# Performance work log

Hardware: AMD Instinct MI355X
Metric: run time of the kernel (lower is better)

Reference implementation:

```python
import jax, jax.numpy as jnp
import numpy as np

B, S, HID, NH = 2, 2048, 1024, 16
HD = HID // NH
BASE = 10000.0


def _rope_tables(seq_len, head_dim):
    i = jnp.arange(0, head_dim, 2, dtype=jnp.float32)
    theta = BASE ** (-i / head_dim)
    pos = jnp.arange(seq_len, dtype=jnp.float32)
    m_theta = jnp.outer(pos, theta)  # [S, HD/2]
    cos = jnp.repeat(jnp.cos(m_theta), 2, axis=1)  # [S, HD]
    sin = jnp.repeat(jnp.sin(m_theta), 2, axis=1)
    return cos, sin


def _apply_rope(x, cos, sin):
    # x: [B, NH, S, HD]; interleaved rotation: (-x1, x0, -x3, x2, ...)
    x_even = x[..., 0::2]
    x_odd = x[..., 1::2]
    inv_x = jnp.stack((-x_odd, x_even), axis=-1).reshape(x.shape)
    return x * cos[None, None] + inv_x * sin[None, None]


def setup_inputs() -> dict:
    key = jax.random.key(0)
    ks = jax.random.split(key, 7)
    q = jax.random.normal(ks[0], (B, S, HID), dtype=jnp.float32)
    k = jax.random.normal(ks[1], (B, S, HID), dtype=jnp.float32)
    v = jax.random.normal(ks[2], (B, S, HID), dtype=jnp.float32)
    scale = 1.0 / np.sqrt(HID)
    Wq = jax.random.normal(ks[3], (HID, HID), dtype=jnp.float32) * scale
    Wk = jax.random.normal(ks[4], (HID, HID), dtype=jnp.float32) * scale
    Wv = jax.random.normal(ks[5], (HID, HID), dtype=jnp.float32) * scale
    Wo = jax.random.normal(ks[6], (HID, HID), dtype=jnp.float32) * scale
    mask = jnp.triu(jnp.ones((S, S), dtype=bool), k=1)[None, None]  # causal, True = masked
    return {"q": q, "k": k, "v": v, "mask": mask,
            "Wq": Wq, "Wk": Wk, "Wv": Wv, "Wo": Wo}


def reference(q, k, v, mask, Wq, Wk, Wv, Wo):
    cos, sin = _rope_tables(S, HD)
    # Linear (torch stores weight as [out, in]; y = x @ W.T)
    qh = (q @ Wq.T).reshape(B, S, NH, HD).transpose(0, 2, 1, 3)
    kh = (k @ Wk.T).reshape(B, S, NH, HD).transpose(0, 2, 1, 3)
    vh = (v @ Wv.T).reshape(B, S, NH, HD).transpose(0, 2, 1, 3)
    qh = _apply_rope(qh, cos, sin)
    kh = _apply_rope(kh, cos, sin)
    scores = jnp.einsum("bhqd,bhkd->bhqk", qh, kh) / np.sqrt(HD)
    neg_min = jnp.finfo(jnp.float32).min
    scores = jnp.where(mask, neg_min, scores)
    attn = jax.nn.softmax(scores, axis=-1)
    out = jnp.einsum("bhqk,bhkd->bhqd", attn, vh)  # [B,NH,S,HD]
    out = out.transpose(0, 2, 1, 3).reshape(B, S, HID)
    return out @ Wo.T
```

## Files before the change

kernel.cpp:

```cpp
#include <hip/hip_runtime.h>

#define S_LEN 2048
#define HIDN  1024
#define NHEAD 16
#define HDIM  64
#define MROWS 4096
#define KDIM  1024
#define NDIM  1024

typedef __attribute__((ext_vector_type(8))) short bf16x8;
typedef __attribute__((ext_vector_type(4))) short bf16x4;
typedef __attribute__((ext_vector_type(4))) float f32x4;

static __device__ __forceinline__ ushort f2bf(float f) {
    unsigned int u = __float_as_uint(f);
    u = (u + 0x7fffu + ((u >> 16) & 1u)) >> 16;
    return (ushort)u;
}
static __device__ __forceinline__ float bf2f(ushort u) {
    return __uint_as_float(((unsigned int)u) << 16);
}

static __device__ __forceinline__ void gload16(const ushort* g, ushort* l) {
    __builtin_amdgcn_global_load_lds(
        (const __attribute__((address_space(1))) unsigned int*)g,
        (__attribute__((address_space(3))) unsigned int*)l, 16, 0, 0);
}

__global__ __launch_bounds__(256) void prep_kernel(
    const float* __restrict__ q, const float* __restrict__ k,
    const float* __restrict__ v, const float* __restrict__ Wq,
    const float* __restrict__ Wk, const float* __restrict__ Wv,
    const float* __restrict__ Wo,
    ushort* __restrict__ qb, ushort* __restrict__ kb, ushort* __restrict__ vb,
    ushort* __restrict__ Wqb, ushort* __restrict__ Wkb, ushort* __restrict__ Wvb,
    ushort* __restrict__ Wob,
    float* __restrict__ rc, float* __restrict__ rs)
{
    const long Q4 = (long)MROWS * KDIM / 4;
    const long W4 = (long)NDIM * KDIM / 4;
    if (blockIdx.x < 16384) {
        long i = (long)blockIdx.x * 256 + threadIdx.x;
        const float* src; ushort* dst; long off;
        if (i < Q4)          { src = q; dst = qb; off = i; }
        else if (i < 2 * Q4) { src = k; dst = kb; off = i - Q4; }
        else if (i < 3 * Q4) { src = v; dst = vb; off = i - 2 * Q4; }
        else {
            long t = i - 3 * Q4;
            int wsel = (int)(t >> 18);
            off = t & (W4 - 1);
            src = (wsel == 0) ? Wq : (wsel == 1) ? Wk : (wsel == 2) ? Wv : Wo;
            dst = (wsel == 0) ? Wqb : (wsel == 1) ? Wkb : (wsel == 2) ? Wvb : Wob;
        }
        float4 vv = ((const float4*)src)[off];
        ushort4 o;
        o.x = f2bf(vv.x); o.y = f2bf(vv.y); o.z = f2bf(vv.z); o.w = f2bf(vv.w);
        ((ushort4*)dst)[off] = o;
    } else {
        int idx = (blockIdx.x - 16384) * 256 + threadIdx.x;
        int s  = idx >> 5;
        int jp = idx & 31;
        float theta = expf(-(float)(2 * jp) * (9.210340371976184f / 64.0f));
        float ang = (float)s * theta;
        float sv, cv;
        sincosf(ang, &sv, &cv);
        rc[idx] = cv;
        rs[idx] = sv;
    }
}

static __device__ __forceinline__ void gemm_mainloop(
    const ushort* __restrict__ A, const ushort* __restrict__ W,
    ushort* As, ushort* Bs, f32x4 (&acc)[2][4],
    int m0, int n0, int tid)
{
    const int lane = tid & 63, wid = tid >> 6;
    const int wm = wid & 1, wn = wid >> 1;
    const int quad = lane >> 4, l15 = lane & 15;

    for (int k0 = 0; k0 < KDIM; k0 += 64) {
        __syncthreads();
#pragma unroll
        for (int rr = 0; rr < 2; ++rr) {
            int sidx = tid + rr * 256;
            int row = sidx >> 3;
            int g = (sidx & 7) ^ (row & 7);
            gload16(A + (size_t)(m0 + row) * KDIM + k0 + g * 8, As + sidx * 8);
        }
#pragma unroll
        for (int rr = 0; rr < 4; ++rr) {
            int sidx = tid + rr * 256;
            int row = sidx >> 3;
            int g = (sidx & 7) ^ (row & 7);
            gload16(W + (size_t)(n0 + row) * KDIM + k0 + g * 8, Bs + sidx * 8);
        }
        __syncthreads();

#pragma unroll
        for (int ks = 0; ks < 2; ++ks) {
            bf16x8 af[2], bfr[4];
#pragma unroll
            for (int i = 0; i < 2; ++i) {
                int row = wm * 32 + i * 16 + l15;
                int gg = ((ks << 2) | quad) ^ (row & 7);
                af[i] = *(const bf16x8*)&As[row * 64 + gg * 8];
            }
#pragma unroll
            for (int j = 0; j < 4; ++j) {
                int row = wn * 64 + j * 16 + l15;
                int gg = ((ks << 2) | quad) ^ (row & 7);
                bfr[j] = *(const bf16x8*)&Bs[row * 64 + gg * 8];
            }
#pragma unroll
            for (int i = 0; i < 2; ++i)
#pragma unroll
                for (int j = 0; j < 4; ++j)
                    acc[i][j] = __builtin_amdgcn_mfma_f32_16x16x32_bf16(
                        af[i], bfr[j], acc[i][j], 0, 0, 0);
        }
    }
}

__global__ __launch_bounds__(256) void gemm_qkv(
    const ushort* __restrict__ qb, const ushort* __restrict__ kb,
    const ushort* __restrict__ vb,
    const ushort* __restrict__ Wqb, const ushort* __restrict__ Wkb,
    const ushort* __restrict__ Wvb,
    ushort* __restrict__ Qh, ushort* __restrict__ Kh, ushort* __restrict__ Vt,
    const float* __restrict__ rc, const float* __restrict__ rs)
{
    __shared__ __align__(16) ushort As[64 * 64];
    __shared__ __align__(16) ushort Bs[128 * 64];

    const int tid = threadIdx.x;
    const int lane = tid & 63, wid = tid >> 6;
    const int wm = wid & 1, wn = wid >> 1;
    const int quad = lane >> 4, l15 = lane & 15;
    const int z = blockIdx.z;

    const ushort* A; const ushort* W; int m0, n0;
    if (z == 2) {
        m0 = ((int)blockIdx.y * 2 + ((int)blockIdx.x >> 5)) * 64;
        n0 = ((int)blockIdx.x & 31) * 128;
        A = Wvb; W = vb;
    } else {
        m0 = blockIdx.x * 64; n0 = blockIdx.y * 128;
        A = (z == 0) ? qb : kb;
        W = (z == 0) ? Wqb : Wkb;
    }

    f32x4 acc[2][4];
#pragma unroll
    for (int i = 0; i < 2; ++i)
#pragma unroll
        for (int j = 0; j < 4; ++j) acc[i][j] = 0.0f;

    gemm_mainloop(A, W, As, Bs, acc, m0, n0, tid);

    if (z != 2) {
        ushort* out = (z == 0) ? Qh : Kh;
        const float scale = (z == 0) ? 0.18033688011112042f : 1.0f;
#pragma unroll
        for (int i = 0; i < 2; ++i)
#pragma unroll
            for (int j = 0; j < 4; ++j)
#pragma unroll
                for (int r = 0; r < 4; ++r) {
                    int m = m0 + wm * 32 + i * 16 + quad * 4 + r;
                    int n = n0 + wn * 64 + j * 16 + l15;
                    float v = acc[i][j][r];
                    int b = m >> 11, s = m & (S_LEN - 1);
                    int h = n >> 6, d = n & 63;
                    int pidx = s * 32 + (d >> 1);
                    float cv = rc[pidx], sv = rs[pidx];
                    float partner = __shfl_xor(v, 1);
                    v = (d & 1) ? (v * cv + partner * sv)
                                : (v * cv - partner * sv);
                    out[((size_t)((b * NHEAD + h) * S_LEN + s)) * HDIM + d] =
                        f2bf(v * scale);
                }
    } else {
#pragma unroll
        for (int i = 0; i < 2; ++i)
#pragma unroll
            for (int j = 0; j < 4; ++j)
#pragma unroll
                for (int r = 0; r < 4; ++r) {
                    int m = m0 + wm * 32 + i * 16 + quad * 4 + r;
                    int n = n0 + wn * 64 + j * 16 + l15;
                    int h = m >> 6, d = m & 63;
                    int b = n >> 11, s = n & (S_LEN - 1);
                    Vt[((size_t)((b * NHEAD + h) * HDIM + d)) * S_LEN + s] =
                        f2bf(acc[i][j][r]);
                }
    }
}

__global__ __launch_bounds__(256) void gemm_out(
    const ushort* __restrict__ O0, const ushort* __restrict__ O1,
    const float* __restrict__ L0, const float* __restrict__ L1,
    const ushort* __restrict__ W, float* __restrict__ out)
{
    __shared__ __align__(16) ushort As[64 * 64];
    __shared__ __align__(16) ushort Bs[128 * 64];

    const int tid = threadIdx.x;
    const int lane = tid & 63, wid = tid >> 6;
    const int wm = wid & 1, wn = wid >> 1;
    const int quad = lane >> 4, l15 = lane & 15;
    const int m0 = blockIdx.x * 64, n0 = blockIdx.y * 128;

    f32x4 acc[2][4];
#pragma unroll
    for (int i = 0; i < 2; ++i)
#pragma unroll
        for (int j = 0; j < 4; ++j) acc[i][j] = 0.0f;

    for (int k0 = 0; k0 < KDIM; k0 += 64) {
        const int h = k0 >> 6;
        bf16x8 a0[2], a1[2];
        float li[2];
#pragma unroll
        for (int rr = 0; rr < 2; ++rr) {
            int sidx = tid + rr * 256;
            int row = sidx >> 3;
            int g = (sidx & 7) ^ (row & 7);
            int m = m0 + row, bb = m >> 11, s = m & (S_LEN - 1);
            size_t rowO = (size_t)(bb * NHEAD + h) * S_LEN + s;
            a0[rr] = *(const bf16x8*)(O0 + rowO * HDIM + g * 8);
            a1[rr] = *(const bf16x8*)(O1 + rowO * HDIM + g * 8);
            li[rr] = __builtin_amdgcn_rcpf(L0[rowO] + L1[rowO]);
        }
        __syncthreads();
#pragma unroll
        for (int rr = 0; rr < 2; ++rr) {
            int sidx = tid + rr * 256;
            bf16x8 packed;
#pragma unroll
            for (int e = 0; e < 8; ++e) {
                float f = (bf2f((ushort)a0[rr][e]) + bf2f((ushort)a1[rr][e])) * li[rr];
                packed[e] = (short)(__float_as_uint(f) >> 16);
            }
            *(bf16x8*)&As[sidx * 8] = packed;
        }
#pragma unroll
        for (int rr = 0; rr < 4; ++rr) {
            int sidx = tid + rr * 256;
            int row = sidx >> 3;
            int g = (sidx & 7) ^ (row & 7);
            gload16(W + (size_t)(n0 + row) * KDIM + k0 + g * 8, Bs + sidx * 8);
        }
        __syncthreads();

#pragma unroll
        for (int ks = 0; ks < 2; ++ks) {
            bf16x8 af[2], bfr[4];
#pragma unroll
            for (int i = 0; i < 2; ++i) {
                int row = wm * 32 + i * 16 + l15;
                int gg = ((ks << 2) | quad) ^ (row & 7);
                af[i] = *(const bf16x8*)&As[row * 64 + gg * 8];
            }
#pragma unroll
            for (int j = 0; j < 4; ++j) {
                int row = wn * 64 + j * 16 + l15;
                int gg = ((ks << 2) | quad) ^ (row & 7);
                bfr[j] = *(const bf16x8*)&Bs[row * 64 + gg * 8];
            }
#pragma unroll
            for (int i = 0; i < 2; ++i)
#pragma unroll
                for (int j = 0; j < 4; ++j)
                    acc[i][j] = __builtin_amdgcn_mfma_f32_16x16x32_bf16(
                        af[i], bfr[j], acc[i][j], 0, 0, 0);
        }
    }

#pragma unroll
    for (int i = 0; i < 2; ++i)
#pragma unroll
        for (int j = 0; j < 4; ++j)
#pragma unroll
            for (int r = 0; r < 4; ++r) {
                int m = m0 + wm * 32 + i * 16 + quad * 4 + r;
                int n = n0 + wn * 64 + j * 16 + l15;
                out[(size_t)m * NDIM + n] = acc[i][j][r];
            }
}

__global__ __launch_bounds__(256) void attn_mfma(
    const ushort* __restrict__ Qh, const ushort* __restrict__ Kh,
    const ushort* __restrict__ Vt,
    ushort* __restrict__ O0, ushort* __restrict__ O1,
    float* __restrict__ L0, float* __restrict__ L1)
{
    __shared__ __align__(16) ushort Ks[64 * 64];
    __shared__ __align__(16) ushort Vs[64 * 64];

    const int tid = threadIdx.x;
    const int lane = tid & 63, w = tid >> 6;
    const int quad = lane >> 4, l15 = lane & 15;
    const int id = blockIdx.x;
    const int h = id & 15, b = (id >> 4) & 1, t = id >> 5;

    int seg, y;
    if (t < 32) { seg = (t & 1) ? 0 : 1; y = (t & 1) ? 31 - (t >> 1) : (t >> 1); }
    else { int u = t - 32; seg = (u & 1) ? 0 : 1;
           y = (u & 1) ? 15 - (u >> 1) : 16 + (u >> 1); }

    const int qt = seg ? (31 - y) : y;
    const int lo = seg ? ((33 - y) >> 1) : 0;
    const int hi = seg ? (32 - y) : ((y + 2) >> 1);
    const int q0 = qt * 64;
    const size_t hoff = (size_t)(b * NHEAD + h) * S_LEN * HDIM;

    bf16x8 qf[2];
#pragma unroll
    for (int ks = 0; ks < 2; ++ks)
        qf[ks] = *(const bf16x8*)(Qh + hoff +
            (size_t)(q0 + w * 16 + l15) * HDIM + ks * 32 + quad * 8);

    f32x4 Oa[4];
#pragma unroll
    for (int mt = 0; mt < 4; ++mt) Oa[mt] = 0.0f;
    float lsum = 0.f;
    const int myq = q0 + w * 16 + l15;

    const ushort* kg[2]; const ushort* vg[2];
#pragma unroll
    for (int rr = 0; rr < 2; ++rr) {
        int sidx = tid + rr * 256;
        int row = sidx >> 3;
        int gsw = (sidx & 7) ^ (row & 7);
        kg[rr] = Kh + hoff + (size_t)(lo * 64 + row) * HDIM + gsw * 8;
        vg[rr] = Vt + hoff + (size_t)row * S_LEN + lo * 64 + gsw * 8;
    }

    for (int kt = lo; kt < hi; ++kt) {
        const int k0 = kt * 64;
        const bool diag = (kt == qt);
        __syncthreads();
#pragma unroll
        for (int rr = 0; rr < 2; ++rr) {
            int sidx = tid + rr * 256;
            gload16(kg[rr], Ks + sidx * 8);
            gload16(vg[rr], Vs + sidx * 8);
            kg[rr] += 64 * HDIM;
            vg[rr] += 64;
        }
        __syncthreads();

        f32x4 Sa[4];
#pragma unroll
        for (int jm = 0; jm < 4; ++jm) Sa[jm] = 0.0f;
#pragma unroll
        for (int ks = 0; ks < 2; ++ks) {
            const int p = ((ks << 2) | quad) ^ (l15 & 7);
            bf16x8 kf[4];
#pragma unroll
            for (int jm = 0; jm < 4; ++jm)
                kf[jm] = *(const bf16x8*)&Ks[(jm * 16 + l15) * 64 + p * 8];
#pragma unroll
            for (int jm = 0; jm < 4; ++jm)
                Sa[jm] = __builtin_amdgcn_mfma_f32_16x16x32_bf16(kf[jm], qf[ks],
                                                                 Sa[jm], 0, 0, 0);
        }

        bf16x4 pb[4];
#pragma unroll
        for (int jm = 0; jm < 4; ++jm) {
#pragma unroll
            for (int r = 0; r < 4; ++r) {
                float pv = __builtin_amdgcn_exp2f(Sa[jm][r]);
                if (diag) {
                    int key = k0 + jm * 16 + quad * 4 + r;
                    if (key > myq) pv = 0.f;
                }
                lsum += pv;
                pb[jm][r] = (short)(__float_as_uint(pv) >> 16);
            }
        }

#pragma unroll
        for (int jm = 0; jm < 4; ++jm) {
            const int off = (((jm * 2 + (quad >> 1)) ^ (l15 & 7)) << 3) + (quad & 1) * 4;
#pragma unroll
            for (int mt = 0; mt < 4; ++mt) {
                bf16x4 vf = *(const bf16x4*)&Vs[(mt * 16 + l15) * 64 + off];
                Oa[mt] = __builtin_amdgcn_mfma_f32_16x16x16bf16_1k(vf, pb[jm],
                                                                   Oa[mt], 0, 0, 0);
            }
        }
    }

    lsum += __shfl_xor(lsum, 16);
    lsum += __shfl_xor(lsum, 32);

    ushort* Op = seg ? O1 : O0;
    float*  Lp = seg ? L1 : L0;
    const size_t row = (size_t)(b * NHEAD + h) * S_LEN + myq;
#pragma unroll
    for (int mt = 0; mt < 4; ++mt) {
        ushort4 o;
        o.x = f2bf(Oa[mt][0]); o.y = f2bf(Oa[mt][1]);
        o.z = f2bf(Oa[mt][2]); o.w = f2bf(Oa[mt][3]);
        *(ushort4*)&Op[row * HDIM + mt * 16 + quad * 4] = o;
    }
    if (quad == 0) Lp[row] = lsum;
}

extern "C" void kernel_launch(void* const* d_in, const int* in_sizes, int n_in,
                              void* d_out, int out_size, void* d_ws, size_t ws_size,
                              hipStream_t stream) {
    const float* qf  = (const float*)d_in[0];
    const float* kf  = (const float*)d_in[1];
    const float* vf  = (const float*)d_in[2];
    const float* Wqf = (const float*)d_in[4];
    const float* Wkf = (const float*)d_in[5];
    const float* Wvf = (const float*)d_in[6];
    const float* Wof = (const float*)d_in[7];
    float* out = (float*)d_out;

    char* wsp = (char*)d_ws;
    float* rc = (float*)wsp;            wsp += 65536 * 4;
    float* rs = (float*)wsp;            wsp += 65536 * 4;
    ushort* qb  = (ushort*)wsp;         wsp += (size_t)MROWS * KDIM * 2;
    ushort* kb  = (ushort*)wsp;         wsp += (size_t)MROWS * KDIM * 2;
    ushort* vb  = (ushort*)wsp;         wsp += (size_t)MROWS * KDIM * 2;
    ushort* Wqb = (ushort*)wsp;         wsp += (size_t)NDIM * KDIM * 2;
    ushort* Wkb = (ushort*)wsp;         wsp += (size_t)NDIM * KDIM * 2;
    ushort* Wvb = (ushort*)wsp;         wsp += (size_t)NDIM * KDIM * 2;
    ushort* Wob = (ushort*)wsp;         wsp += (size_t)NDIM * KDIM * 2;
    ushort* Qh  = (ushort*)wsp;         wsp += (size_t)MROWS * HIDN * 2;
    ushort* Kh  = (ushort*)wsp;         wsp += (size_t)MROWS * HIDN * 2;
    ushort* Vt  = (ushort*)wsp;

    ushort* O0 = qb;
    ushort* O1 = kb;
    float*  L0 = (float*)vb;
    float*  L1 = (float*)vb + 65536;

    prep_kernel<<<16640, 256, 0, stream>>>(qf, kf, vf, Wqf, Wkf, Wvf, Wof,
                                           qb, kb, vb, Wqb, Wkb, Wvb, Wob, rc, rs);

    gemm_qkv<<<dim3(64, 8, 3), 256, 0, stream>>>(
        qb, kb, vb, Wqb, Wkb, Wvb, Qh, Kh, Vt, rc, rs);

    attn_mfma<<<2048, 256, 0, stream>>>(Qh, Kh, Vt, O0, O1, L0, L1);

    gemm_out<<<dim3(64, 8), 256, 0, stream>>>(O0, O1, L0, L1, Wob, out);
}
```

Baseline: 208.0 us.

## Enlarge QKV GEMM tile to 128x128 and register-prefetch V with 8-byte swizzle

The QKV projection GEMM moves from 64x128 to 128x128 block tiles, with each wave computing a 4x4 grid of MFMA tiles, halving the grid and adding an occupancy hint of 3 blocks. This raises operand reuse per LDS load and cuts global traffic for the weight and activation tiles. In attention, V tiles are now prefetched one step ahead into registers and written to LDS with a finer 4-element XOR swizzle that matches the 16x16x16 MFMA read pattern. This aims to reduce LDS bank conflicts on V reads and hide V load latency, at the cost of extra registers and fewer blocks for the GEMM.

```diff
diff --git a/kernel.cpp b/kernel.cpp
--- a/kernel.cpp
+++ b/kernel.cpp
@@ -69,9 +69,9 @@
     }
 }
 
-static __device__ __forceinline__ void gemm_mainloop(
+static __device__ __forceinline__ void gemm_mainloop128(
     const ushort* __restrict__ A, const ushort* __restrict__ W,
-    ushort* As, ushort* Bs, f32x4 (&acc)[2][4],
+    ushort* As, ushort* Bs, f32x4 (&acc)[4][4],
     int m0, int n0, int tid)
 {
     const int lane = tid & 63, wid = tid >> 6;
@@ -81,27 +81,21 @@
     for (int k0 = 0; k0 < KDIM; k0 += 64) {
         __syncthreads();
 #pragma unroll
-        for (int rr = 0; rr < 2; ++rr) {
+        for (int rr = 0; rr < 4; ++rr) {
             int sidx = tid + rr * 256;
             int row = sidx >> 3;
             int g = (sidx & 7) ^ (row & 7);
             gload16(A + (size_t)(m0 + row) * KDIM + k0 + g * 8, As + sidx * 8);
-        }
-#pragma unroll
-        for (int rr = 0; rr < 4; ++rr) {
-            int sidx = tid + rr * 256;
-            int row = sidx >> 3;
-            int g = (sidx & 7) ^ (row & 7);
             gload16(W + (size_t)(n0 + row) * KDIM + k0 + g * 8, Bs + sidx * 8);
         }
         __syncthreads();
 
 #pragma unroll
         for (int ks = 0; ks < 2; ++ks) {
-            bf16x8 af[2], bfr[4];
-#pragma unroll
-            for (int i = 0; i < 2; ++i) {
-                int row = wm * 32 + i * 16 + l15;
+            bf16x8 af[4], bfr[4];
+#pragma unroll
+            for (int i = 0; i < 4; ++i) {
+                int row = wm * 64 + i * 16 + l15;
                 int gg = ((ks << 2) | quad) ^ (row & 7);
                 af[i] = *(const bf16x8*)&As[row * 64 + gg * 8];
             }
@@ -112,7 +106,7 @@
                 bfr[j] = *(const bf16x8*)&Bs[row * 64 + gg * 8];
             }
 #pragma unroll
-            for (int i = 0; i < 2; ++i)
+            for (int i = 0; i < 4; ++i)
 #pragma unroll
                 for (int j = 0; j < 4; ++j)
                     acc[i][j] = __builtin_amdgcn_mfma_f32_16x16x32_bf16(
@@ -121,7 +115,7 @@
     }
 }
 
-__global__ __launch_bounds__(256) void gemm_qkv(
+__global__ __launch_bounds__(256, 3) void gemm_qkv(
     const ushort* __restrict__ qb, const ushort* __restrict__ kb,
     const ushort* __restrict__ vb,
     const ushort* __restrict__ Wqb, const ushort* __restrict__ Wkb,
@@ -129,7 +123,7 @@
     ushort* __restrict__ Qh, ushort* __restrict__ Kh, ushort* __restrict__ Vt,
     const float* __restrict__ rc, const float* __restrict__ rs)
 {
-    __shared__ __align__(16) ushort As[64 * 64];
+    __shared__ __align__(16) ushort As[128 * 64];
     __shared__ __align__(16) ushort Bs[128 * 64];
 
     const int tid = threadIdx.x;
@@ -140,33 +134,33 @@
 
     const ushort* A; const ushort* W; int m0, n0;
     if (z == 2) {
-        m0 = ((int)blockIdx.y * 2 + ((int)blockIdx.x >> 5)) * 64;
-        n0 = ((int)blockIdx.x & 31) * 128;
+        m0 = (int)blockIdx.y * 128;
+        n0 = (int)blockIdx.x * 128;
         A = Wvb; W = vb;
     } else {
-        m0 = blockIdx.x * 64; n0 = blockIdx.y * 128;
+        m0 = blockIdx.x * 128; n0 = blockIdx.y * 128;
         A = (z == 0) ? qb : kb;
         W = (z == 0) ? Wqb : Wkb;
     }
 
-    f32x4 acc[2][4];
-#pragma unroll
-    for (int i = 0; i < 2; ++i)
+    f32x4 acc[4][4];
+#pragma unroll
+    for (int i = 0; i < 4; ++i)
 #pragma unroll
         for (int j = 0; j < 4; ++j) acc[i][j] = 0.0f;
 
-    gemm_mainloop(A, W, As, Bs, acc, m0, n0, tid);
+    gemm_mainloop128(A, W, As, Bs, acc, m0, n0, tid);
 
     if (z != 2) {
         ushort* out = (z == 0) ? Qh : Kh;
         const float scale = (z == 0) ? 0.18033688011112042f : 1.0f;
 #pragma unroll
-        for (int i = 0; i < 2; ++i)
+        for (int i = 0; i < 4; ++i)
 #pragma unroll
             for (int j = 0; j < 4; ++j)
 #pragma unroll
                 for (int r = 0; r < 4; ++r) {
-                    int m = m0 + wm * 32 + i * 16 + quad * 4 + r;
+                    int m = m0 + wm * 64 + i * 16 + quad * 4 + r;
                     int n = n0 + wn * 64 + j * 16 + l15;
                     float v = acc[i][j][r];
                     int b = m >> 11, s = m & (S_LEN - 1);
@@ -181,12 +175,12 @@
                 }
     } else {
 #pragma unroll
-        for (int i = 0; i < 2; ++i)
+        for (int i = 0; i < 4; ++i)
 #pragma unroll
             for (int j = 0; j < 4; ++j)
 #pragma unroll
                 for (int r = 0; r < 4; ++r) {
-                    int m = m0 + wm * 32 + i * 16 + quad * 4 + r;
+                    int m = m0 + wm * 64 + i * 16 + quad * 4 + r;
                     int n = n0 + wn * 64 + j * 16 + l15;
                     int h = m >> 6, d = m & 63;
                     int b = n >> 11, s = n & (S_LEN - 1);
@@ -326,14 +320,25 @@
     float lsum = 0.f;
     const int myq = q0 + w * 16 + l15;
 
-    const ushort* kg[2]; const ushort* vg[2];
+    const ushort* kg[2];
+    const ushort* vgr[2];
+    int vwa[2][2];
 #pragma unroll
     for (int rr = 0; rr < 2; ++rr) {
         int sidx = tid + rr * 256;
         int row = sidx >> 3;
         int gsw = (sidx & 7) ^ (row & 7);
         kg[rr] = Kh + hoff + (size_t)(lo * 64 + row) * HDIM + gsw * 8;
-        vg[rr] = Vt + hoff + (size_t)row * S_LEN + lo * 64 + gsw * 8;
+        int sp = sidx & 7;
+        vgr[rr] = Vt + hoff + (size_t)row * S_LEN + lo * 64 + sp * 8;
+        vwa[rr][0] = row * 64 + ((2 * sp)     ^ (row & 15)) * 4;
+        vwa[rr][1] = row * 64 + ((2 * sp + 1) ^ (row & 15)) * 4;
+    }
+
+    bf16x8 vv[2];
+    if (lo < hi) {
+#pragma unroll
+        for (int rr = 0; rr < 2; ++rr) { vv[rr] = *(const bf16x8*)vgr[rr]; vgr[rr] += 64; }
     }
 
     for (int kt = lo; kt < hi; ++kt) {
@@ -342,11 +347,16 @@
         __syncthreads();
 #pragma unroll
         for (int rr = 0; rr < 2; ++rr) {
-            int sidx = tid + rr * 256;
-            gload16(kg[rr], Ks + sidx * 8);
-            gload16(vg[rr], Vs + sidx * 8);
+            *(bf16x4*)&Vs[vwa[rr][0]] =
+                __builtin_shufflevector(vv[rr], vv[rr], 0, 1, 2, 3);
+            *(bf16x4*)&Vs[vwa[rr][1]] =
+                __builtin_shufflevector(vv[rr], vv[rr], 4, 5, 6, 7);
+            gload16(kg[rr], Ks + (tid + rr * 256) * 8);
             kg[rr] += 64 * HDIM;
-            vg[rr] += 64;
+        }
+        if (kt + 1 < hi) {
+#pragma unroll
+            for (int rr = 0; rr < 2; ++rr) { vv[rr] = *(const bf16x8*)vgr[rr]; vgr[rr] += 64; }
         }
         __syncthreads();
 
@@ -383,10 +393,10 @@
 
 #pragma unroll
         for (int jm = 0; jm < 4; ++jm) {
-            const int off = (((jm * 2 + (quad >> 1)) ^ (l15 & 7)) << 3) + (quad & 1) * 4;
+            const int slot = (((jm * 4 + quad) ^ l15) << 2);
 #pragma unroll
             for (int mt = 0; mt < 4; ++mt) {
-                bf16x4 vf = *(const bf16x4*)&Vs[(mt * 16 + l15) * 64 + off];
+                bf16x4 vf = *(const bf16x4*)&Vs[(mt * 16 + l15) * 64 + slot];
                 Oa[mt] = __builtin_amdgcn_mfma_f32_16x16x16bf16_1k(vf, pb[jm],
                                                                    Oa[mt], 0, 0, 0);
             }
@@ -443,7 +453,7 @@
     prep_kernel<<<16640, 256, 0, stream>>>(qf, kf, vf, Wqf, Wkf, Wvf, Wof,
                                            qb, kb, vb, Wqb, Wkb, Wvb, Wob, rc, rs);
 
-    gemm_qkv<<<dim3(64, 8, 3), 256, 0, stream>>>(
+    gemm_qkv<<<dim3(32, 8, 3), 256, 0, stream>>>(
         qb, kb, vb, Wqb, Wkb, Wvb, Qh, Kh, Vt, rc, rs);
 
     attn_mfma<<<2048, 256, 0, stream>>>(Qh, Kh, Vt, O0, O1, L0, L1);
```

Measured after the change: 214.7 us. +3.2%, slower.
